# Optimization experiments

Hardware: AMD Instinct MI355X
Metric: run time of the kernel (lower is better)

The kernel has to match this reference:

```python
import jax, jax.numpy as jnp
import numpy as np

N = 100000      # nodes
E = 800000      # edges (avg degree 8)
F = 5           # num_node_features
D = 128         # embed_dim
H = 4           # heads
HD = D // H     # per-head dim = 32
H1, H2 = 64, 128  # mlp hidden dims


def _mlp(x, W1, b1, W2, b2, W3, b3):
    h = jax.nn.relu(x @ W1 + b1)
    h = jax.nn.relu(h @ W2 + b2)
    return h @ W3 + b3


def setup_inputs() -> dict:
    key = jax.random.key(0)
    ks = jax.random.split(key, 24)
    g = lambda i, shape: (jax.random.normal(ks[i], shape, dtype=jnp.float32) * 0.05)
    z = lambda d: jnp.zeros((d,), dtype=jnp.float32)
    return {
        "x": jax.random.normal(ks[0], (N, F), dtype=jnp.float32),
        "edge_index": jax.random.randint(ks[1], (2, E), 0, N),
        # mlp_prep: F -> 64 -> 128 -> D
        "prep_W1": g(2, (F, H1)),  "prep_b1": z(H1),
        "prep_W2": g(3, (H1, H2)), "prep_b2": z(H2),
        "prep_W3": g(4, (H2, D)),  "prep_b3": z(D),
        # mlp_update: D -> 64 -> 128 -> D
        "upd_W1": g(5, (D, H1)),   "upd_b1": z(H1),
        "upd_W2": g(6, (H1, H2)),  "upd_b2": z(H2),
        "upd_W3": g(7, (H2, D)),   "upd_b3": z(D),
        # TransformerConv projections (heads=4, per-head 32, concat -> D)
        "q_W": g(8, (D, D)),  "q_b": z(D),
        "k_W": g(9, (D, D)),  "k_b": z(D),
        "v_W": g(10, (D, D)), "v_b": z(D),
        "skip_W": g(11, (D, D)), "skip_b": z(D),
    }


def _transformer_conv(x, edge_index, q_W, q_b, k_W, k_b, v_W, v_b, skip_W, skip_b):
    # PyG TransformerConv: messages flow src=edge_index[0] -> dst=edge_index[1]
    src, dst = edge_index[0], edge_index[1]
    q = (x @ q_W + q_b).reshape(N, H, HD)
    k = (x @ k_W + k_b).reshape(N, H, HD)
    v = (x @ v_W + v_b).reshape(N, H, HD)
    scale = 1.0 / np.sqrt(HD).astype(np.float32)
    # per-edge attention logits [E, H]
    score = jnp.einsum('ehd,ehd->eh', q[dst], k[src]) * scale
    # segment softmax over incoming edges of each destination node
    m = jax.ops.segment_max(score, dst, num_segments=N)          # [N, H]
    e = jnp.exp(score - m[dst])                                  # [E, H]
    denom = jax.ops.segment_sum(e, dst, num_segments=N)         # [N, H]
    alpha = e / denom[dst]                                       # [E, H]
    # scatter-aggregate weighted values
    agg = jax.ops.segment_sum(alpha[..., None] * v[src], dst, num_segments=N)  # [N, H, HD]
    return agg.reshape(N, H * HD) + (x @ skip_W + skip_b)


def reference(x, edge_index,
              prep_W1, prep_b1, prep_W2, prep_b2, prep_W3, prep_b3,
              upd_W1, upd_b1, upd_W2, upd_b2, upd_W3, upd_b3,
              q_W, q_b, k_W, k_b, v_W, v_b, skip_W, skip_b):
    h_init = _mlp(x, prep_W1, prep_b1, prep_W2, prep_b2, prep_W3, prep_b3)
    h = _transformer_conv(h_init, edge_index, q_W, q_b, k_W, k_b, v_W, v_b, skip_W, skip_b)
    return h + _mlp(h, upd_W1, upd_b1, upd_W2, upd_b2, upd_W3, upd_b3)
```

## Files before the change

### kernel.cpp

```cpp
#include <hip/hip_runtime.h>
#include <hip/hip_bf16.h>

#define N_  100000
#define F_  5
#define D_  128
#define H_  4
#define HD_ 32
#define E_  800000

typedef __attribute__((ext_vector_type(8))) short bf16x8;
typedef __attribute__((ext_vector_type(4))) float f32x4;

__device__ __forceinline__ unsigned short f2bf(float f) {
  unsigned u = __float_as_uint(f);
  u += 0x7FFF + ((u >> 16) & 1);
  return (unsigned short)(u >> 16);
}

__device__ __forceinline__ unsigned pk2(float a, float b) {
  __hip_bfloat162 h = __float22bfloat162_rn(make_float2(a, b));
  return *(unsigned*)&h;
}

__device__ __forceinline__ float2 bf2f2(unsigned u) {
  float2 r;
  r.x = __uint_as_float(u << 16);
  r.y = __uint_as_float(u & 0xffff0000u);
  return r;
}

__device__ __forceinline__ float rowsum8(float x) {
  x += __int_as_float(__builtin_amdgcn_update_dpp(0, __float_as_int(x), 0x0B1, 0xF, 0xF, false));
  x += __int_as_float(__builtin_amdgcn_update_dpp(0, __float_as_int(x), 0x04E, 0xF, 0xF, false));
  x += __int_as_float(__builtin_amdgcn_update_dpp(0, __float_as_int(x), 0x141, 0xF, 0xF, false));
  return x;
}

template<int K, int M>
__device__ __forceinline__ void wconv_one(const float* __restrict__ W,
                                          unsigned short* __restrict__ WT,
                                          int idx) {
  const int r = idx & 7;
  const int l = (idx >> 3) & 15;
  const int rest = idx >> 7;
  const int kq = rest % (K / 8);
  const int i  = rest / (K / 8);
  WT[idx] = f2bf(W[(kq * 8 + r) * M + i * 16 + l]);
}

#define WCONV_NB 480
#define HIST_NB  ((E_ + 255) / 256)
#define SCAN_NB  ((N_ + 255) / 256)

__global__ __launch_bounds__(256) void k_wconv_hist(
    const float* __restrict__ w0, const float* __restrict__ w1,
    const float* __restrict__ w2, const float* __restrict__ w3,
    const float* __restrict__ w4, const float* __restrict__ w5,
    const float* __restrict__ w6, const float* __restrict__ w7,
    const float* __restrict__ w8, unsigned short* __restrict__ WT,
    const int* __restrict__ ei, int* __restrict__ deg)
{
  if (blockIdx.x >= WCONV_NB) {
    const int e = (blockIdx.x - WCONV_NB) * 256 + threadIdx.x;
    if (e < E_) atomicAdd(&deg[ei[E_ + e]], 1);
    return;
  }
  const int idx = blockIdx.x * 256 + threadIdx.x;
  if (idx < 8192)        wconv_one<64, 128>(w0, WT,          idx);
  else if (idx < 24576)  wconv_one<128,128>(w1, WT + 8192,   idx - 8192);
  else if (idx < 40960)  wconv_one<128,128>(w2, WT + 24576,  idx - 24576);
  else if (idx < 57344)  wconv_one<128,128>(w3, WT + 40960,  idx - 40960);
  else if (idx < 73728)  wconv_one<128,128>(w4, WT + 57344,  idx - 57344);
  else if (idx < 90112)  wconv_one<128,128>(w5, WT + 73728,  idx - 73728);
  else if (idx < 98304)  wconv_one<128, 64>(w6, WT + 90112,  idx - 90112);
  else if (idx < 106496) wconv_one<64, 128>(w7, WT + 98304,  idx - 98304);
  else                   wconv_one<128,128>(w8, WT + 106496, idx - 106496);
}

template<int K, int M>
__device__ __forceinline__ void gemm_frag64(const unsigned short* sX,
                                            const unsigned short* __restrict__ WT,
                                            f32x4 (*acc)[4],
                                            int wr, int l16, int kg)
{
  constexpr int SX = K + 8;
  constexpr int IF = M / 64;
  #pragma unroll
  for (int i = 0; i < IF; ++i)
    #pragma unroll
    for (int j = 0; j < 4; ++j) acc[i][j] = (f32x4){0.f, 0.f, 0.f, 0.f};
  #pragma unroll
  for (int k0 = 0; k0 < K; k0 += 32) {
    const int kq = k0 / 8 + kg;
    bf16x8 aw[IF];
    #pragma unroll
    for (int i = 0; i < IF; ++i)
      aw[i] = *(const bf16x8*)&WT[(((wr * IF + i) * (K / 8) + kq) * 16 + l16) * 8];
    #pragma unroll
    for (int j = 0; j < 4; ++j) {
      const bf16x8 bx = *(const bf16x8*)&sX[(j * 16 + l16) * SX + k0 + kg * 8];
      #pragma unroll
      for (int i = 0; i < IF; ++i)
        acc[i][j] = __builtin_amdgcn_mfma_f32_16x16x32_bf16(aw[i], bx, acc[i][j], 0, 0, 0);
    }
  }
}

template<int M, bool RELU, int SXO>
__device__ __forceinline__ void acc_to_lds64(unsigned short* sY, f32x4 (*acc)[4],
                                             const float* __restrict__ bias,
                                             int wr, int l16, int kg)
{
  constexpr int IF = M / 64;
  float4 b4[IF];
  #pragma unroll
  for (int i = 0; i < IF; ++i)
    b4[i] = *(const float4*)&bias[(wr * IF + i) * 16 + kg * 4];
  #pragma unroll
  for (int j = 0; j < 4; ++j) {
    const int row = j * 16 + l16;
    #pragma unroll
    for (int i = 0; i < IF; ++i) {
      const int f0 = (wr * IF + i) * 16 + kg * 4;
      float ox = acc[i][j][0] + b4[i].x, oy = acc[i][j][1] + b4[i].y;
      float oz = acc[i][j][2] + b4[i].z, ow = acc[i][j][3] + b4[i].w;
      if constexpr (RELU) {
        ox = fmaxf(ox, 0.f); oy = fmaxf(oy, 0.f);
        oz = fmaxf(oz, 0.f); ow = fmaxf(ow, 0.f);
      }
      uint2 p;
      p.x = pk2(ox, oy);
      p.y = pk2(oz, ow);
      *(uint2*)&sY[row * SXO + f0] = p;
    }
  }
}

__global__ __launch_bounds__(256) void k_scan1(const int* __restrict__ deg,
                                               int* __restrict__ off,
                                               int* __restrict__ bsum) {
  __shared__ int s[256];
  const int t = threadIdx.x;
  const int i = blockIdx.x * 256 + t;
  const int v = (i < N_) ? deg[i] : 0;
  s[t] = v;
  __syncthreads();
  #pragma unroll
  for (int o = 1; o < 256; o <<= 1) {
    int u = (t >= o) ? s[t - o] : 0;
    __syncthreads();
    s[t] += u;
    __syncthreads();
  }
  if (i < N_) off[i] = s[t] - v;
  if (t == 255) bsum[blockIdx.x] = s[255];
}

__global__ __launch_bounds__(256) void k_scan23(const int* __restrict__ off,
                                                const int* __restrict__ bsum,
                                                int* __restrict__ cur,
                                                const int* __restrict__ deg,
                                                int2* __restrict__ meta) {
  __shared__ int sacc[256];
  const int t = threadIdx.x;
  const int bid = blockIdx.x;
  int s = 0;
  for (int j = t; j < bid; j += 256) s += bsum[j];
  sacc[t] = s;
  __syncthreads();
  #pragma unroll
  for (int o = 128; o > 0; o >>= 1) {
    if (t < o) sacc[t] += sacc[t + o];
    __syncthreads();
  }
  const int prefix = sacc[0];
  const int i = bid * 256 + t;
  if (i < N_) {
    const int o = off[i] + prefix;
    cur[i] = o;
    meta[i] = make_int2(o, deg[i]);
  }
}

__global__ __launch_bounds__(256) void k_fill_prep(
    const int* __restrict__ ei, int* __restrict__ cur, int* __restrict__ esrc,
    const float* __restrict__ x,
    const float* __restrict__ pW1, const float* __restrict__ pb1,
    const unsigned short* __restrict__ wt_p2, const float* __restrict__ pb2,
    const unsigned short* __restrict__ wt_p3, const float* __restrict__ pb3,
    const unsigned short* __restrict__ wt_q, const float* __restrict__ qb,
    const unsigned short* __restrict__ wt_k, const float* __restrict__ kb,
    const unsigned short* __restrict__ wt_v, const float* __restrict__ vb,
    const unsigned short* __restrict__ wt_s, const float* __restrict__ sb,
    unsigned short* __restrict__ q16, unsigned short* __restrict__ k16,
    unsigned short* __restrict__ v16, float* __restrict__ out)
{
  __shared__ __align__(16) unsigned short bufA[64 * 72];
  __shared__ __align__(16) unsigned short bufB[64 * 136];

  const int bmod = blockIdx.x % 3;
  if (bmod != 2) {
    const int fid = (blockIdx.x / 3) * 2 + bmod;
    const int e = fid * 256 + threadIdx.x;
    if (e < E_) {
      const int src = ei[e], dst = ei[E_ + e];
      const int pos = atomicAdd(&cur[dst], 1);
      esrc[pos] = src;
    }
    return;
  }

  const int t = threadIdx.x;
  const int node0 = (blockIdx.x / 3) * 64;
  const int lane = t & 63;
  const int wr = t >> 6;
  const int l16 = lane & 15, kg = lane >> 4;

  float* sxs = (float*)bufB;
  float* sw1 = (float*)bufB + 320;
  {
    const long gbase = (long)node0 * F_;
    for (int i = t; i < 64 * F_; i += 256) {
      const long g = gbase + i;
      sxs[i] = (g < (long)N_ * F_) ? x[g] : 0.f;
    }
    for (int i = t; i < 384; i += 256)
      sw1[i] = (i < 320) ? pW1[i] : pb1[i - 320];
  }
  __syncthreads();

  {
    const int n = t >> 2;
    const int f0b = (t & 3) * 16;
    float xr[F_];
    #pragma unroll
    for (int k = 0; k < F_; ++k) xr[k] = sxs[n * F_ + k];
    const float* sb1 = sw1 + 320;
    #pragma unroll
    for (int q = 0; q < 4; ++q) {
      float o[4];
      #pragma unroll
      for (int jj = 0; jj < 4; ++jj) {
        const int f = f0b + q * 4 + jj;
        float a = sb1[f];
        #pragma unroll
        for (int k = 0; k < F_; ++k) a = fmaf(xr[k], sw1[k * 64 + f], a);
        o[jj] = fmaxf(a, 0.f);
      }
      uint2 pkd;
      pkd.x = pk2(o[0], o[1]);
      pkd.y = pk2(o[2], o[3]);
      *(uint2*)&bufA[n * 72 + f0b + q * 4] = pkd;
    }
  }
  __syncthreads();

  f32x4 acc[2][4];

  gemm_frag64<64, 128>(bufA, wt_p2, acc, wr, l16, kg);
  acc_to_lds64<128, true, 136>(bufB, acc, pb2, wr, l16, kg);
  __syncthreads();

  gemm_frag64<128, 128>(bufB, wt_p3, acc, wr, l16, kg);
  __syncthreads();
  acc_to_lds64<128, false, 136>(bufB, acc, pb3, wr, l16, kg);
  __syncthreads();

  {
    const unsigned short* wtsP[3] = {wt_q, wt_k, wt_v};
    const float* bsP[3] = {qb, kb, vb};
    unsigned short* ysP[3] = {q16, k16, v16};
    #pragma unroll
    for (int ws = 0; ws < 3; ++ws) {
      gemm_frag64<128, 128>(bufB, wtsP[ws], acc, wr, l16, kg);
      const float* __restrict__ bias = bsP[ws];
      unsigned short* __restrict__ Yb = ysP[ws];
      float4 b4[2];
      #pragma unroll
      for (int i = 0; i < 2; ++i)
        b4[i] = *(const float4*)&bias[(wr * 2 + i) * 16 + kg * 4];
      #pragma unroll
      for (int j = 0; j < 4; ++j) {
        const int node = node0 + j * 16 + l16;
        if (node >= N_) continue;
        #pragma unroll
        for (int i = 0; i < 2; ++i) {
          const int f0 = (wr * 2 + i) * 16 + kg * 4;
          uint2 ob;
          ob.x = pk2(acc[i][j][0] + b4[i].x, acc[i][j][1] + b4[i].y);
          ob.y = pk2(acc[i][j][2] + b4[i].z, acc[i][j][3] + b4[i].w);
          *(uint2*)&Yb[(long)node * D_ + f0] = ob;
        }
      }
    }
  }

  gemm_frag64<128, 128>(bufB, wt_s, acc, wr, l16, kg);
  {
    float4 b4[2];
    #pragma unroll
    for (int i = 0; i < 2; ++i)
      b4[i] = *(const float4*)&sb[(wr * 2 + i) * 16 + kg * 4];
    #pragma unroll
    for (int j = 0; j < 4; ++j) {
      const int node = node0 + j * 16 + l16;
      if (node >= N_) continue;
      #pragma unroll
      for (int i = 0; i < 2; ++i) {
        const int f0 = (wr * 2 + i) * 16 + kg * 4;
        float4 o = make_float4(acc[i][j][0] + b4[i].x, acc[i][j][1] + b4[i].y,
                               acc[i][j][2] + b4[i].z, acc[i][j][3] + b4[i].w);
        *(float4*)&out[(long)node * D_ + f0] = o;
      }
    }
  }
}

__global__ __launch_bounds__(256) void k_update(
    const unsigned short* __restrict__ wt_u1, const float* __restrict__ ub1,
    const unsigned short* __restrict__ wt_u2, const float* __restrict__ ub2,
    const unsigned short* __restrict__ wt_u3, const float* __restrict__ ub3,
    float* __restrict__ out)
{
  __shared__ __align__(16) unsigned short bufA[64 * 72];
  __shared__ __align__(16) unsigned short bufB[64 * 136];

  const int t = threadIdx.x;
  const int node0 = blockIdx.x * 64;
  const int lane = t & 63;
  const int wr = t >> 6;
  const int l16 = lane & 15, kg = lane >> 4;

  #pragma unroll
  for (int i = 0; i < 8; ++i) {
    const int g = t + 256 * i;
    const int row = g >> 5;
    const int kc  = g & 31;
    const int node = node0 + row;
    float4 xv = (node < N_) ? ((const float4*)out)[(long)node * 32 + kc]
                            : make_float4(0.f, 0.f, 0.f, 0.f);
    uint2 p;
    p.x = pk2(xv.x, xv.y);
    p.y = pk2(xv.z, xv.w);
    *(uint2*)&bufB[row * 136 + kc * 4] = p;
  }
  __syncthreads();

  f32x4 acc[2][4];

  gemm_frag64<128, 64>(bufB, wt_u1, acc, wr, l16, kg);
  acc_to_lds64<64, true, 72>(bufA, acc, ub1, wr, l16, kg);
  __syncthreads();

  gemm_frag64<64, 128>(bufA, wt_u2, acc, wr, l16, kg);
  acc_to_lds64<128, true, 136>(bufB, acc, ub2, wr, l16, kg);
  __syncthreads();

  gemm_frag64<128, 128>(bufB, wt_u3, acc, wr, l16, kg);
  {
    float4 b4[2];
    #pragma unroll
    for (int i = 0; i < 2; ++i)
      b4[i] = *(const float4*)&ub3[(wr * 2 + i) * 16 + kg * 4];
    #pragma unroll
    for (int j = 0; j < 4; ++j) {
      const int node = node0 + j * 16 + l16;
      if (node >= N_) continue;
      #pragma unroll
      for (int i = 0; i < 2; ++i) {
        const int f0 = (wr * 2 + i) * 16 + kg * 4;
        const float4 r = *(const float4*)&out[(long)node * D_ + f0];
        float4 o = make_float4(acc[i][j][0] + b4[i].x + r.x,
                               acc[i][j][1] + b4[i].y + r.y,
                               acc[i][j][2] + b4[i].z + r.z,
                               acc[i][j][3] + b4[i].w + r.w);
        *(float4*)&out[(long)node * D_ + f0] = o;
      }
    }
  }
}

__global__ __launch_bounds__(256) void k_attn(
    const int* __restrict__ esrc, const int2* __restrict__ meta,
    const unsigned short* __restrict__ q,
    const unsigned short* __restrict__ kbuf,
    const unsigned short* __restrict__ vbuf,
    float* __restrict__ out)
{
  const int t = threadIdx.x;
  const unsigned node = blockIdx.x * 8 + (t >> 5);
  const int c = t & 31;
  const float C = 0.17677669529663687f * 1.4426950408889634f;

  const int2 md = meta[node];
  const int start = md.x, cnt = md.y;
  const int end = start + cnt;

  const uint2 qu = *(const uint2*)&q[(node << 7) + 4u * c];
  const float2 q01 = bf2f2(qu.x), q23 = bf2f2(qu.y);
  const float qx0 = q01.x * C, qx1 = q01.y * C;
  const float qx2 = q23.x * C, qx3 = q23.y * C;

  float l = 0.f, a0 = 0.f, a1 = 0.f, a2 = 0.f, a3 = 0.f;

  const int P = (cnt + 1) >> 1;
  if (P > 0) {
    bool v1c = (start + 1) < end;
    unsigned i0 = esrc[start];
    unsigned i1 = esrc[v1c ? start + 1 : start];
    uint2 kA = *(const uint2*)&kbuf[((long)i0 << 7) + 4u * c];
    uint2 kB = *(const uint2*)&kbuf[((long)i1 << 7) + 4u * c];
    uint2 wA = *(const uint2*)&vbuf[((long)i0 << 7) + 4u * c];
    uint2 wB = *(const uint2*)&vbuf[((long)i1 << 7) + 4u * c];
    bool v0n = (start + 2) < end, v1n = (start + 3) < end;
    unsigned i0n = esrc[v0n ? start + 2 : start];
    unsigned i1n = esrc[v1n ? start + 3 : start];

    for (int it = 0;;) {
      const bool more = (it + 1) < P;
      uint2 kAn, kBn, wAn, wBn;
      unsigned i0f = 0, i1f = 0;
      bool v0f = false, v1f = false;
      if (more) {
        kAn = *(const uint2*)&kbuf[((long)i0n << 7) + 4u * c];
        kBn = *(const uint2*)&kbuf[((long)i1n << 7) + 4u * c];
        wAn = *(const uint2*)&vbuf[((long)i0n << 7) + 4u * c];
        wBn = *(const uint2*)&vbuf[((long)i1n << 7) + 4u * c];
        const int ef = start + 2 * (it + 2);
        v0f = ef < end; v1f = (ef + 1) < end;
        i0f = esrc[v0f ? ef : start];
        i1f = esrc[v1f ? ef + 1 : start];
      }

      const float2 ka01 = bf2f2(kA.x), ka23 = bf2f2(kA.y);
      const float2 kb01 = bf2f2(kB.x), kb23 = bf2f2(kB.y);
      float sA = fmaf(qx0, ka01.x, fmaf(qx1, ka01.y, fmaf(qx2, ka23.x, qx3 * ka23.y)));
      float sB = fmaf(qx0, kb01.x, fmaf(qx1, kb01.y, fmaf(qx2, kb23.x, qx3 * kb23.y)));
      sA = rowsum8(sA);
      sB = rowsum8(sB);
      const float eA = __builtin_amdgcn_exp2f(sA);
      const float eB = v1c ? __builtin_amdgcn_exp2f(sB) : 0.f;
      const float2 va01 = bf2f2(wA.x), va23 = bf2f2(wA.y);
      const float2 vb01 = bf2f2(wB.x), vb23 = bf2f2(wB.y);
      l += eA + eB;
      a0 = fmaf(eA, va01.x, fmaf(eB, vb01.x, a0));
      a1 = fmaf(eA, va01.y, fmaf(eB, vb01.y, a1));
      a2 = fmaf(eA, va23.x, fmaf(eB, vb23.x, a2));
      a3 = fmaf(eA, va23.y, fmaf(eB, vb23.y, a3));

      if (!more) break;
      ++it;
      kA = kAn; kB = kBn; wA = wAn; wB = wBn;
      v1c = v1n;
      v0n = v0f; v1n = v1f;
      i0n = i0f; i1n = i1f;
    }
  }

  if (l > 0.f) {
    const float inv = 1.0f / l;
    float4* op = (float4*)&out[(node << 7) + 4u * c];
    float4 cv = *op;
    cv.x += a0 * inv;
    cv.y += a1 * inv;
    cv.z += a2 * inv;
    cv.w += a3 * inv;
    *op = cv;
  }
}

extern "C" void kernel_launch(void* const* d_in, const int* in_sizes, int n_in,
                              void* d_out, int out_size, void* d_ws, size_t ws_size,
                              hipStream_t stream) {
  const float* x   = (const float*)d_in[0];
  const int*   ei  = (const int*)d_in[1];
  const float* pW1 = (const float*)d_in[2];  const float* pb1 = (const float*)d_in[3];
  const float* pW2 = (const float*)d_in[4];  const float* pb2 = (const float*)d_in[5];
  const float* pW3 = (const float*)d_in[6];  const float* pb3 = (const float*)d_in[7];
  const float* uW1 = (const float*)d_in[8];  const float* ub1 = (const float*)d_in[9];
  const float* uW2 = (const float*)d_in[10]; const float* ub2 = (const float*)d_in[11];
  const float* uW3 = (const float*)d_in[12]; const float* ub3 = (const float*)d_in[13];
  const float* qW  = (const float*)d_in[14]; const float* qb  = (const float*)d_in[15];
  const float* kW  = (const float*)d_in[16]; const float* kb  = (const float*)d_in[17];
  const float* vW  = (const float*)d_in[18]; const float* vb  = (const float*)d_in[19];
  const float* sW  = (const float*)d_in[20]; const float* sb  = (const float*)d_in[21];

  float* out = (float*)d_out;
  float* ws  = (float*)d_ws;

  const long ND = (long)N_ * D_;
  unsigned short* q16 = (unsigned short*)(ws + ND);
  unsigned short* k16 = (unsigned short*)(ws + 2 * ND);
  unsigned short* v16 = (unsigned short*)(ws + 3 * ND);

  unsigned short* wtb = (unsigned short*)(ws + 4 * ND);
  unsigned short* wt_p2 = wtb;
  unsigned short* wt_p3 = wtb + 8192;
  unsigned short* wt_q  = wtb + 24576;
  unsigned short* wt_k  = wtb + 40960;
  unsigned short* wt_v  = wtb + 57344;
  unsigned short* wt_s  = wtb + 73728;
  unsigned short* wt_u1 = wtb + 90112;
  unsigned short* wt_u2 = wtb + 98304;
  unsigned short* wt_u3 = wtb + 106496;

  int* deg  = (int*)ws;
  int* off  = deg + N_;
  int* cur  = off + N_;
  int* esrc = cur + N_;
  int* bsum = esrc + E_;
  int2* meta = (int2*)(bsum + 512);

  const int gT64 = (N_ + 63) / 64;

  hipMemsetAsync(deg, 0, N_ * sizeof(int), stream);

  k_wconv_hist<<<WCONV_NB + HIST_NB, 256, 0, stream>>>(
      pW2, pW3, qW, kW, vW, sW, uW1, uW2, uW3, wtb, ei, deg);

  k_scan1 <<<SCAN_NB, 256, 0, stream>>>(deg, off, bsum);
  k_scan23<<<SCAN_NB, 256, 0, stream>>>(off, bsum, cur, deg, meta);

  k_fill_prep<<<3 * gT64, 256, 0, stream>>>(
      ei, cur, esrc,
      x, pW1, pb1, wt_p2, pb2, wt_p3, pb3,
      wt_q, qb, wt_k, kb, wt_v, vb, wt_s, sb,
      q16, k16, v16, out);

  k_attn<<<N_ / 8, 256, 0, stream>>>(esrc, meta, q16, k16, v16, out);

  k_update<<<gT64, 256, 0, stream>>>(wt_u1, ub1, wt_u2, ub2, wt_u3, ub3, out);
}
```

Measured before the change: 314.9 us.

## Overlap attention tail with update MLP and write bf16 h for update

```diff
diff --git a/kernel.cpp b/kernel.cpp
--- a/kernel.cpp
+++ b/kernel.cpp
@@ -7,6 +7,8 @@
 #define H_  4
 #define HD_ 32
 #define E_  800000
+
+#define NA_ 50048
 
 typedef __attribute__((ext_vector_type(8))) short bf16x8;
 typedef __attribute__((ext_vector_type(4))) float f32x4;
@@ -182,8 +184,9 @@
   }
 }
 
-__global__ __launch_bounds__(256) void k_fill_prep(
-    const int* __restrict__ ei, int* __restrict__ cur, int* __restrict__ esrc,
+__device__ __forceinline__ void prep_body(
+    int node0, int t,
+    unsigned short* bufA, unsigned short* bufB,
     const float* __restrict__ x,
     const float* __restrict__ pW1, const float* __restrict__ pb1,
     const unsigned short* __restrict__ wt_p2, const float* __restrict__ pb2,
@@ -195,23 +198,6 @@
     unsigned short* __restrict__ q16, unsigned short* __restrict__ k16,
     unsigned short* __restrict__ v16, float* __restrict__ out)
 {
-  __shared__ __align__(16) unsigned short bufA[64 * 72];
-  __shared__ __align__(16) unsigned short bufB[64 * 136];
-
-  const int bmod = blockIdx.x % 3;
-  if (bmod != 2) {
-    const int fid = (blockIdx.x / 3) * 2 + bmod;
-    const int e = fid * 256 + threadIdx.x;
-    if (e < E_) {
-      const int src = ei[e], dst = ei[E_ + e];
-      const int pos = atomicAdd(&cur[dst], 1);
-      esrc[pos] = src;
-    }
-    return;
-  }
-
-  const int t = threadIdx.x;
-  const int node0 = (blockIdx.x / 3) * 64;
   const int lane = t & 63;
   const int wr = t >> 6;
   const int l16 = lane & 15, kg = lane >> 4;
@@ -316,87 +302,53 @@
   }
 }
 
-__global__ __launch_bounds__(256) void k_update(
-    const unsigned short* __restrict__ wt_u1, const float* __restrict__ ub1,
-    const unsigned short* __restrict__ wt_u2, const float* __restrict__ ub2,
-    const unsigned short* __restrict__ wt_u3, const float* __restrict__ ub3,
-    float* __restrict__ out)
+__global__ __launch_bounds__(256) void k_fill_prep(
+    const int* __restrict__ ei, int* __restrict__ cur, int* __restrict__ esrc,
+    const float* __restrict__ x,
+    const float* __restrict__ pW1, const float* __restrict__ pb1,
+    const unsigned short* __restrict__ wt_p2, const float* __restrict__ pb2,
+    const unsigned short* __restrict__ wt_p3, const float* __restrict__ pb3,
+    const unsigned short* __restrict__ wt_q, const float* __restrict__ qb,
+    const unsigned short* __restrict__ wt_k, const float* __restrict__ kb,
+    const unsigned short* __restrict__ wt_v, const float* __restrict__ vb,
+    const unsigned short* __restrict__ wt_s, const float* __restrict__ sb,
+    unsigned short* __restrict__ q16, unsigned short* __restrict__ k16,
+    unsigned short* __restrict__ v16, float* __restrict__ out)
 {
   __shared__ __align__(16) unsigned short bufA[64 * 72];
   __shared__ __align__(16) unsigned short bufB[64 * 136];
 
-  const int t = threadIdx.x;
-  const int node0 = blockIdx.x * 64;
-  const int lane = t & 63;
-  const int wr = t >> 6;
-  const int l16 = lane & 15, kg = lane >> 4;
-
-  #pragma unroll
-  for (int i = 0; i < 8; ++i) {
-    const int g = t + 256 * i;
-    const int row = g >> 5;
-    const int kc  = g & 31;
-    const int node = node0 + row;
-    float4 xv = (node < N_) ? ((const float4*)out)[(long)node * 32 + kc]
-                            : make_float4(0.f, 0.f, 0.f, 0.f);
-    uint2 p;
-    p.x = pk2(xv.x, xv.y);
-    p.y = pk2(xv.z, xv.w);
-    *(uint2*)&bufB[row * 136 + kc * 4] = p;
-  }
-  __syncthreads();
-
-  f32x4 acc[2][4];
-
-  gemm_frag64<128, 64>(bufB, wt_u1, acc, wr, l16, kg);
-  acc_to_lds64<64, true, 72>(bufA, acc, ub1, wr, l16, kg);
-  __syncthreads();
-
-  gemm_frag64<64, 128>(bufA, wt_u2, acc, wr, l16, kg);
-  acc_to_lds64<128, true, 136>(bufB, acc, ub2, wr, l16, kg);
-  __syncthreads();
-
-  gemm_frag64<128, 128>(bufB, wt_u3, acc, wr, l16, kg);
-  {
-    float4 b4[2];
-    #pragma unroll
-    for (int i = 0; i < 2; ++i)
-      b4[i] = *(const float4*)&ub3[(wr * 2 + i) * 16 + kg * 4];
-    #pragma unroll
-    for (int j = 0; j < 4; ++j) {
-      const int node = node0 + j * 16 + l16;
-      if (node >= N_) continue;
-      #pragma unroll
-      for (int i = 0; i < 2; ++i) {
-        const int f0 = (wr * 2 + i) * 16 + kg * 4;
-        const float4 r = *(const float4*)&out[(long)node * D_ + f0];
-        float4 o = make_float4(acc[i][j][0] + b4[i].x + r.x,
-                               acc[i][j][1] + b4[i].y + r.y,
-                               acc[i][j][2] + b4[i].z + r.z,
-                               acc[i][j][3] + b4[i].w + r.w);
-        *(float4*)&out[(long)node * D_ + f0] = o;
-      }
-    }
-  }
-}
-
-__global__ __launch_bounds__(256) void k_attn(
+  const int bmod = blockIdx.x % 3;
+  if (bmod != 2) {
+    const int fid = (blockIdx.x / 3) * 2 + bmod;
+    const int e = fid * 256 + threadIdx.x;
+    if (e < E_) {
+      const int src = ei[e], dst = ei[E_ + e];
+      const int pos = atomicAdd(&cur[dst], 1);
+      esrc[pos] = src;
+    }
+    return;
+  }
+  prep_body((blockIdx.x / 3) * 64, threadIdx.x, bufA, bufB,
+            x, pW1, pb1, wt_p2, pb2, wt_p3, pb3,
+            wt_q, qb, wt_k, kb, wt_v, vb, wt_s, sb,
+            q16, k16, v16, out);
+}
+
+__device__ __forceinline__ void attn_node(
+    unsigned node, int c,
     const int* __restrict__ esrc, const int2* __restrict__ meta,
-    const unsigned short* __restrict__ q,
+    unsigned short* __restrict__ q16,
     const unsigned short* __restrict__ kbuf,
     const unsigned short* __restrict__ vbuf,
     float* __restrict__ out)
 {
-  const int t = threadIdx.x;
-  const unsigned node = blockIdx.x * 8 + (t >> 5);
-  const int c = t & 31;
   const float C = 0.17677669529663687f * 1.4426950408889634f;
-
   const int2 md = meta[node];
   const int start = md.x, cnt = md.y;
   const int end = start + cnt;
 
-  const uint2 qu = *(const uint2*)&q[(node << 7) + 4u * c];
+  const uint2 qu = *(const uint2*)&q16[((long)node << 7) + 4u * c];
   const float2 q01 = bf2f2(qu.x), q23 = bf2f2(qu.y);
   const float qx0 = q01.x * C, qx1 = q01.y * C;
   const float qx2 = q23.x * C, qx3 = q23.y * C;
@@ -457,16 +409,131 @@
     }
   }
 
+  float r0 = 0.f, r1 = 0.f, r2 = 0.f, r3 = 0.f;
   if (l > 0.f) {
     const float inv = 1.0f / l;
-    float4* op = (float4*)&out[(node << 7) + 4u * c];
-    float4 cv = *op;
-    cv.x += a0 * inv;
-    cv.y += a1 * inv;
-    cv.z += a2 * inv;
-    cv.w += a3 * inv;
-    *op = cv;
-  }
+    r0 = a0 * inv; r1 = a1 * inv; r2 = a2 * inv; r3 = a3 * inv;
+  }
+
+  float4* op = (float4*)&out[((long)node << 7) + 4u * c];
+  float4 sk = *op;
+  const float h0 = sk.x + r0, h1 = sk.y + r1;
+  const float h2 = sk.z + r2, h3 = sk.w + r3;
+  *op = make_float4(h0, h1, h2, h3);
+  uint2 hb;
+  hb.x = pk2(h0, h1);
+  hb.y = pk2(h2, h3);
+  *(uint2*)&q16[((long)node << 7) + 4u * c] = hb;
+}
+
+__global__ __launch_bounds__(256) void k_attn(
+    const int* __restrict__ esrc, const int2* __restrict__ meta,
+    unsigned short* __restrict__ q16,
+    const unsigned short* __restrict__ kbuf,
+    const unsigned short* __restrict__ vbuf,
+    float* __restrict__ out, int node0)
+{
+  const int t = threadIdx.x;
+  attn_node(node0 + blockIdx.x * 8 + (t >> 5), t & 31,
+            esrc, meta, q16, kbuf, vbuf, out);
+}
+
+__device__ __forceinline__ void update_body(
+    int node0, int t,
+    unsigned short* bufA, unsigned short* bufB,
+    const unsigned short* __restrict__ h16,
+    const unsigned short* __restrict__ wt_u1, const float* __restrict__ ub1,
+    const unsigned short* __restrict__ wt_u2, const float* __restrict__ ub2,
+    const unsigned short* __restrict__ wt_u3, const float* __restrict__ ub3,
+    float* __restrict__ out)
+{
+  const int lane = t & 63;
+  const int wr = t >> 6;
+  const int l16 = lane & 15, kg = lane >> 4;
+
+  #pragma unroll
+  for (int i = 0; i < 4; ++i) {
+    const int g = t + 256 * i;
+    const int row = g >> 4;
+    const int kc  = g & 15;
+    const int node = node0 + row;
+    uint4 v = (node < N_) ? *(const uint4*)&h16[((long)node << 7) + kc * 8]
+                          : make_uint4(0u, 0u, 0u, 0u);
+    *(uint4*)&bufB[row * 136 + kc * 8] = v;
+  }
+  __syncthreads();
+
+  f32x4 acc[2][4];
+
+  gemm_frag64<128, 64>(bufB, wt_u1, acc, wr, l16, kg);
+  acc_to_lds64<64, true, 72>(bufA, acc, ub1, wr, l16, kg);
+  __syncthreads();
+
+  gemm_frag64<64, 128>(bufA, wt_u2, acc, wr, l16, kg);
+  acc_to_lds64<128, true, 136>(bufB, acc, ub2, wr, l16, kg);
+  __syncthreads();
+
+  gemm_frag64<128, 128>(bufB, wt_u3, acc, wr, l16, kg);
+  {
+    float4 b4[2];
+    #pragma unroll
+    for (int i = 0; i < 2; ++i)
+      b4[i] = *(const float4*)&ub3[(wr * 2 + i) * 16 + kg * 4];
+    #pragma unroll
+    for (int j = 0; j < 4; ++j) {
+      const int node = node0 + j * 16 + l16;
+      if (node >= N_) continue;
+      #pragma unroll
+      for (int i = 0; i < 2; ++i) {
+        const int f0 = (wr * 2 + i) * 16 + kg * 4;
+        const float4 r = *(const float4*)&out[(long)node * D_ + f0];
+        float4 o = make_float4(acc[i][j][0] + b4[i].x + r.x,
+                               acc[i][j][1] + b4[i].y + r.y,
+                               acc[i][j][2] + b4[i].z + r.z,
+                               acc[i][j][3] + b4[i].w + r.w);
+        *(float4*)&out[(long)node * D_ + f0] = o;
+      }
+    }
+  }
+}
+
+__global__ __launch_bounds__(256) void k_attnB_updA(
+    const int* __restrict__ esrc, const int2* __restrict__ meta,
+    unsigned short* __restrict__ q16,
+    const unsigned short* __restrict__ kbuf,
+    const unsigned short* __restrict__ vbuf,
+    const unsigned short* __restrict__ wt_u1, const float* __restrict__ ub1,
+    const unsigned short* __restrict__ wt_u2, const float* __restrict__ ub2,
+    const unsigned short* __restrict__ wt_u3, const float* __restrict__ ub3,
+    float* __restrict__ out)
+{
+  __shared__ __align__(16) unsigned short bufA[64 * 72];
+  __shared__ __align__(16) unsigned short bufB[64 * 136];
+
+  const int bid = blockIdx.x;
+  const int t = threadIdx.x;
+  if (bid % 9 == 8) {
+    update_body((bid / 9) * 64, t, bufA, bufB, q16,
+                wt_u1, ub1, wt_u2, ub2, wt_u3, ub3, out);
+    return;
+  }
+  const int aid = (bid / 9) * 8 + (bid % 9);
+  if (aid >= (N_ - NA_) / 8) return;
+  attn_node(NA_ + aid * 8 + (t >> 5), t & 31,
+            esrc, meta, q16, kbuf, vbuf, out);
+}
+
+__global__ __launch_bounds__(256) void k_update(
+    const unsigned short* __restrict__ h16,
+    const unsigned short* __restrict__ wt_u1, const float* __restrict__ ub1,
+    const unsigned short* __restrict__ wt_u2, const float* __restrict__ ub2,
+    const unsigned short* __restrict__ wt_u3, const float* __restrict__ ub3,
+    float* __restrict__ out, int node0)
+{
+  __shared__ __align__(16) unsigned short bufA[64 * 72];
+  __shared__ __align__(16) unsigned short bufB[64 * 136];
+  update_body(node0 + blockIdx.x * 64, threadIdx.x, bufA, bufB, h16,
+              wt_u1, ub1, wt_u2, ub2, wt_u3, ub3, out);
 }
 
 extern "C" void kernel_launch(void* const* d_in, const int* in_sizes, int n_in,
@@ -527,7 +594,12 @@
       wt_q, qb, wt_k, kb, wt_v, vb, wt_s, sb,
       q16, k16, v16, out);
 
-  k_attn<<<N_ / 8, 256, 0, stream>>>(esrc, meta, q16, k16, v16, out);
-
-  k_update<<<gT64, 256, 0, stream>>>(wt_u1, ub1, wt_u2, ub2, wt_u3, ub3, out);
-}
+  k_attn<<<NA_ / 8, 256, 0, stream>>>(esrc, meta, q16, k16, v16, out, 0);
+
+  k_attnB_updA<<<9 * (NA_ / 64), 256, 0, stream>>>(
+      esrc, meta, q16, k16, v16,
+      wt_u1, ub1, wt_u2, ub2, wt_u3, ub3, out);
+
+  k_update<<<(N_ - NA_ + 63) / 64, 256, 0, stream>>>(
+      q16, wt_u1, ub1, wt_u2, ub2, wt_u3, ub3, out, NA_);
+}
```

Result: no change. 319.0 us (+1.3%).

## Spread prep MLP tiles across scan kernels and pass bf16 h to update

Applied to the files above, without the earlier changes.

```diff
diff --git a/kernel.cpp b/kernel.cpp
--- a/kernel.cpp
+++ b/kernel.cpp
@@ -51,6 +51,8 @@
 #define WCONV_NB 480
 #define HIST_NB  ((E_ + 255) / 256)
 #define SCAN_NB  ((N_ + 255) / 256)
+#define PREP_NT  1563
+#define PREP_CH  521
 
 __global__ __launch_bounds__(256) void k_wconv_hist(
     const float* __restrict__ w0, const float* __restrict__ w1,
@@ -136,54 +138,9 @@
   }
 }
 
-__global__ __launch_bounds__(256) void k_scan1(const int* __restrict__ deg,
-                                               int* __restrict__ off,
-                                               int* __restrict__ bsum) {
-  __shared__ int s[256];
-  const int t = threadIdx.x;
-  const int i = blockIdx.x * 256 + t;
-  const int v = (i < N_) ? deg[i] : 0;
-  s[t] = v;
-  __syncthreads();
-  #pragma unroll
-  for (int o = 1; o < 256; o <<= 1) {
-    int u = (t >= o) ? s[t - o] : 0;
-    __syncthreads();
-    s[t] += u;
-    __syncthreads();
-  }
-  if (i < N_) off[i] = s[t] - v;
-  if (t == 255) bsum[blockIdx.x] = s[255];
-}
-
-__global__ __launch_bounds__(256) void k_scan23(const int* __restrict__ off,
-                                                const int* __restrict__ bsum,
-                                                int* __restrict__ cur,
-                                                const int* __restrict__ deg,
-                                                int2* __restrict__ meta) {
-  __shared__ int sacc[256];
-  const int t = threadIdx.x;
-  const int bid = blockIdx.x;
-  int s = 0;
-  for (int j = t; j < bid; j += 256) s += bsum[j];
-  sacc[t] = s;
-  __syncthreads();
-  #pragma unroll
-  for (int o = 128; o > 0; o >>= 1) {
-    if (t < o) sacc[t] += sacc[t + o];
-    __syncthreads();
-  }
-  const int prefix = sacc[0];
-  const int i = bid * 256 + t;
-  if (i < N_) {
-    const int o = off[i] + prefix;
-    cur[i] = o;
-    meta[i] = make_int2(o, deg[i]);
-  }
-}
-
-__global__ __launch_bounds__(256) void k_fill_prep(
-    const int* __restrict__ ei, int* __restrict__ cur, int* __restrict__ esrc,
+__device__ __forceinline__ void prep_body(
+    int node0, int t,
+    unsigned short* bufA, unsigned short* bufB,
     const float* __restrict__ x,
     const float* __restrict__ pW1, const float* __restrict__ pb1,
     const unsigned short* __restrict__ wt_p2, const float* __restrict__ pb2,
@@ -195,23 +152,6 @@
     unsigned short* __restrict__ q16, unsigned short* __restrict__ k16,
     unsigned short* __restrict__ v16, float* __restrict__ out)
 {
-  __shared__ __align__(16) unsigned short bufA[64 * 72];
-  __shared__ __align__(16) unsigned short bufB[64 * 136];
-
-  const int bmod = blockIdx.x % 3;
-  if (bmod != 2) {
-    const int fid = (blockIdx.x / 3) * 2 + bmod;
-    const int e = fid * 256 + threadIdx.x;
-    if (e < E_) {
-      const int src = ei[e], dst = ei[E_ + e];
-      const int pos = atomicAdd(&cur[dst], 1);
-      esrc[pos] = src;
-    }
-    return;
-  }
-
-  const int t = threadIdx.x;
-  const int node0 = (blockIdx.x / 3) * 64;
   const int lane = t & 63;
   const int wr = t >> 6;
   const int l16 = lane & 15, kg = lane >> 4;
@@ -316,73 +256,109 @@
   }
 }
 
-__global__ __launch_bounds__(256) void k_update(
-    const unsigned short* __restrict__ wt_u1, const float* __restrict__ ub1,
-    const unsigned short* __restrict__ wt_u2, const float* __restrict__ ub2,
-    const unsigned short* __restrict__ wt_u3, const float* __restrict__ ub3,
-    float* __restrict__ out)
+#define PREP_ARGS                                                        \
+    const float* __restrict__ x,                                         \
+    const float* __restrict__ pW1, const float* __restrict__ pb1,        \
+    const unsigned short* __restrict__ wt_p2, const float* __restrict__ pb2, \
+    const unsigned short* __restrict__ wt_p3, const float* __restrict__ pb3, \
+    const unsigned short* __restrict__ wt_q, const float* __restrict__ qb,   \
+    const unsigned short* __restrict__ wt_k, const float* __restrict__ kb,   \
+    const unsigned short* __restrict__ wt_v, const float* __restrict__ vb,   \
+    const unsigned short* __restrict__ wt_s, const float* __restrict__ sb,   \
+    unsigned short* __restrict__ q16, unsigned short* __restrict__ k16,  \
+    unsigned short* __restrict__ v16, float* __restrict__ out
+
+#define PREP_PASS x, pW1, pb1, wt_p2, pb2, wt_p3, pb3, wt_q, qb, wt_k, kb, \
+                  wt_v, vb, wt_s, sb, q16, k16, v16, out
+
+__global__ __launch_bounds__(256) void k_scan1_prep(
+    const int* __restrict__ deg, int* __restrict__ off, int* __restrict__ bsum,
+    PREP_ARGS)
 {
   __shared__ __align__(16) unsigned short bufA[64 * 72];
   __shared__ __align__(16) unsigned short bufB[64 * 136];
+  __shared__ int s[256];
 
   const int t = threadIdx.x;
-  const int node0 = blockIdx.x * 64;
-  const int lane = t & 63;
-  const int wr = t >> 6;
-  const int l16 = lane & 15, kg = lane >> 4;
-
-  #pragma unroll
-  for (int i = 0; i < 8; ++i) {
-    const int g = t + 256 * i;
-    const int row = g >> 5;
-    const int kc  = g & 31;
-    const int node = node0 + row;
-    float4 xv = (node < N_) ? ((const float4*)out)[(long)node * 32 + kc]
-                            : make_float4(0.f, 0.f, 0.f, 0.f);
-    uint2 p;
-    p.x = pk2(xv.x, xv.y);
-    p.y = pk2(xv.z, xv.w);
-    *(uint2*)&bufB[row * 136 + kc * 4] = p;
-  }
-  __syncthreads();
-
-  f32x4 acc[2][4];
-
-  gemm_frag64<128, 64>(bufB, wt_u1, acc, wr, l16, kg);
-  acc_to_lds64<64, true, 72>(bufA, acc, ub1, wr, l16, kg);
-  __syncthreads();
-
-  gemm_frag64<64, 128>(bufA, wt_u2, acc, wr, l16, kg);
-  acc_to_lds64<128, true, 136>(bufB, acc, ub2, wr, l16, kg);
-  __syncthreads();
-
-  gemm_frag64<128, 128>(bufB, wt_u3, acc, wr, l16, kg);
-  {
-    float4 b4[2];
-    #pragma unroll
-    for (int i = 0; i < 2; ++i)
-      b4[i] = *(const float4*)&ub3[(wr * 2 + i) * 16 + kg * 4];
-    #pragma unroll
-    for (int j = 0; j < 4; ++j) {
-      const int node = node0 + j * 16 + l16;
-      if (node >= N_) continue;
-      #pragma unroll
-      for (int i = 0; i < 2; ++i) {
-        const int f0 = (wr * 2 + i) * 16 + kg * 4;
-        const float4 r = *(const float4*)&out[(long)node * D_ + f0];
-        float4 o = make_float4(acc[i][j][0] + b4[i].x + r.x,
-                               acc[i][j][1] + b4[i].y + r.y,
-                               acc[i][j][2] + b4[i].z + r.z,
-                               acc[i][j][3] + b4[i].w + r.w);
-        *(float4*)&out[(long)node * D_ + f0] = o;
-      }
-    }
-  }
+  if (blockIdx.x < SCAN_NB) {
+    const int i = blockIdx.x * 256 + t;
+    const int v = (i < N_) ? deg[i] : 0;
+    s[t] = v;
+    __syncthreads();
+    #pragma unroll
+    for (int o = 1; o < 256; o <<= 1) {
+      int u = (t >= o) ? s[t - o] : 0;
+      __syncthreads();
+      s[t] += u;
+      __syncthreads();
+    }
+    if (i < N_) off[i] = s[t] - v;
+    if (t == 255) bsum[blockIdx.x] = s[255];
+    return;
+  }
+  prep_body((blockIdx.x - SCAN_NB) * 64, t, bufA, bufB, PREP_PASS);
+}
+
+__global__ __launch_bounds__(256) void k_scan23_prep(
+    const int* __restrict__ off, const int* __restrict__ bsum,
+    int* __restrict__ cur, const int* __restrict__ deg,
+    int2* __restrict__ meta, PREP_ARGS)
+{
+  __shared__ __align__(16) unsigned short bufA[64 * 72];
+  __shared__ __align__(16) unsigned short bufB[64 * 136];
+  __shared__ int sacc[256];
+
+  const int t = threadIdx.x;
+  if (blockIdx.x < SCAN_NB) {
+    const int bid = blockIdx.x;
+    int s = 0;
+    for (int j = t; j < bid; j += 256) s += bsum[j];
+    sacc[t] = s;
+    __syncthreads();
+    #pragma unroll
+    for (int o = 128; o > 0; o >>= 1) {
+      if (t < o) sacc[t] += sacc[t + o];
+      __syncthreads();
+    }
+    const int prefix = sacc[0];
+    const int i = bid * 256 + t;
+    if (i < N_) {
+      const int o = off[i] + prefix;
+      cur[i] = o;
+      meta[i] = make_int2(o, deg[i]);
+    }
+    return;
+  }
+  prep_body((PREP_CH + blockIdx.x - SCAN_NB) * 64, t, bufA, bufB, PREP_PASS);
+}
+
+__global__ __launch_bounds__(256) void k_fill_prep(
+    const int* __restrict__ ei, int* __restrict__ cur, int* __restrict__ esrc,
+    PREP_ARGS)
+{
+  __shared__ __align__(16) unsigned short bufA[64 * 72];
+  __shared__ __align__(16) unsigned short bufB[64 * 136];
+
+  const int t = threadIdx.x;
+  const int bmod = blockIdx.x % 7;
+  if (bmod != 6) {
+    const int fid = (blockIdx.x / 7) * 6 + bmod;
+    const int e = fid * 256 + t;
+    if (e < E_) {
+      const int src = ei[e], dst = ei[E_ + e];
+      const int pos = atomicAdd(&cur[dst], 1);
+      esrc[pos] = src;
+    }
+    return;
+  }
+  const int tile = 2 * PREP_CH + blockIdx.x / 7;
+  if (tile >= PREP_NT) return;
+  prep_body(tile * 64, t, bufA, bufB, PREP_PASS);
 }
 
 __global__ __launch_bounds__(256) void k_attn(
     const int* __restrict__ esrc, const int2* __restrict__ meta,
-    const unsigned short* __restrict__ q,
+    unsigned short* __restrict__ q16,
     const unsigned short* __restrict__ kbuf,
     const unsigned short* __restrict__ vbuf,
     float* __restrict__ out)
@@ -396,7 +372,7 @@
   const int start = md.x, cnt = md.y;
   const int end = start + cnt;
 
-  const uint2 qu = *(const uint2*)&q[(node << 7) + 4u * c];
+  const uint2 qu = *(const uint2*)&q16[((long)node << 7) + 4u * c];
   const float2 q01 = bf2f2(qu.x), q23 = bf2f2(qu.y);
   const float qx0 = q01.x * C, qx1 = q01.y * C;
   const float qx2 = q23.x * C, qx3 = q23.y * C;
@@ -457,15 +433,82 @@
     }
   }
 
+  float r0 = 0.f, r1 = 0.f, r2 = 0.f, r3 = 0.f;
   if (l > 0.f) {
     const float inv = 1.0f / l;
-    float4* op = (float4*)&out[(node << 7) + 4u * c];
-    float4 cv = *op;
-    cv.x += a0 * inv;
-    cv.y += a1 * inv;
-    cv.z += a2 * inv;
-    cv.w += a3 * inv;
-    *op = cv;
+    r0 = a0 * inv; r1 = a1 * inv; r2 = a2 * inv; r3 = a3 * inv;
+  }
+
+  float4* op = (float4*)&out[((long)node << 7) + 4u * c];
+  float4 sk = *op;
+  const float h0 = sk.x + r0, h1 = sk.y + r1;
+  const float h2 = sk.z + r2, h3 = sk.w + r3;
+  *op = make_float4(h0, h1, h2, h3);
+  uint2 hb;
+  hb.x = pk2(h0, h1);
+  hb.y = pk2(h2, h3);
+  *(uint2*)&q16[((long)node << 7) + 4u * c] = hb;
+}
+
+__global__ __launch_bounds__(256) void k_update(
+    const unsigned short* __restrict__ h16,
+    const unsigned short* __restrict__ wt_u1, const float* __restrict__ ub1,
+    const unsigned short* __restrict__ wt_u2, const float* __restrict__ ub2,
+    const unsigned short* __restrict__ wt_u3, const float* __restrict__ ub3,
+    float* __restrict__ out)
+{
+  __shared__ __align__(16) unsigned short bufA[64 * 72];
+  __shared__ __align__(16) unsigned short bufB[64 * 136];
+
+  const int t = threadIdx.x;
+  const int node0 = blockIdx.x * 64;
+  const int lane = t & 63;
+  const int wr = t >> 6;
+  const int l16 = lane & 15, kg = lane >> 4;
+
+  #pragma unroll
+  for (int i = 0; i < 4; ++i) {
+    const int g = t + 256 * i;
+    const int row = g >> 4;
+    const int kc  = g & 15;
+    const int node = node0 + row;
+    uint4 v = (node < N_) ? *(const uint4*)&h16[((long)node << 7) + kc * 8]
+                          : make_uint4(0u, 0u, 0u, 0u);
+    *(uint4*)&bufB[row * 136 + kc * 8] = v;
+  }
+  __syncthreads();
+
+  f32x4 acc[2][4];
+
+  gemm_frag64<128, 64>(bufB, wt_u1, acc, wr, l16, kg);
+  acc_to_lds64<64, true, 72>(bufA, acc, ub1, wr, l16, kg);
+  __syncthreads();
+
+  gemm_frag64<64, 128>(bufA, wt_u2, acc, wr, l16, kg);
+  acc_to_lds64<128, true, 136>(bufB, acc, ub2, wr, l16, kg);
+  __syncthreads();
+
+  gemm_frag64<128, 128>(bufB, wt_u3, acc, wr, l16, kg);
+  {
+    float4 b4[2];
+    #pragma unroll
+    for (int i = 0; i < 2; ++i)
+      b4[i] = *(const float4*)&ub3[(wr * 2 + i) * 16 + kg * 4];
+    #pragma unroll
+    for (int j = 0; j < 4; ++j) {
+      const int node = node0 + j * 16 + l16;
+      if (node >= N_) continue;
+      #pragma unroll
+      for (int i = 0; i < 2; ++i) {
+        const int f0 = (wr * 2 + i) * 16 + kg * 4;
+        const float4 r = *(const float4*)&out[(long)node * D_ + f0];
+        float4 o = make_float4(acc[i][j][0] + b4[i].x + r.x,
+                               acc[i][j][1] + b4[i].y + r.y,
+                               acc[i][j][2] + b4[i].z + r.z,
+                               acc[i][j][3] + b4[i].w + r.w);
+        *(float4*)&out[(long)node * D_ + f0] = o;
+      }
+    }
   }
 }
 
@@ -511,17 +554,24 @@
   int* bsum = esrc + E_;
   int2* meta = (int2*)(bsum + 512);
 
-  const int gT64 = (N_ + 63) / 64;
-
   hipMemsetAsync(deg, 0, N_ * sizeof(int), stream);
 
   k_wconv_hist<<<WCONV_NB + HIST_NB, 256, 0, stream>>>(
       pW2, pW3, qW, kW, vW, sW, uW1, uW2, uW3, wtb, ei, deg);
 
-  k_scan1 <<<SCAN_NB, 256, 0, stream>>>(deg, off, bsum);
-  k_scan23<<<SCAN_NB, 256, 0, stream>>>(off, bsum, cur, deg, meta);
-
-  k_fill_prep<<<3 * gT64, 256, 0, stream>>>(
+  k_scan1_prep<<<SCAN_NB + PREP_CH, 256, 0, stream>>>(
+      deg, off, bsum,
+      x, pW1, pb1, wt_p2, pb2, wt_p3, pb3,
+      wt_q, qb, wt_k, kb, wt_v, vb, wt_s, sb,
+      q16, k16, v16, out);
+
+  k_scan23_prep<<<SCAN_NB + PREP_CH, 256, 0, stream>>>(
+      off, bsum, cur, deg, meta,
+      x, pW1, pb1, wt_p2, pb2, wt_p3, pb3,
+      wt_q, qb, wt_k, kb, wt_v, vb, wt_s, sb,
+      q16, k16, v16, out);
+
+  k_fill_prep<<<7 * (PREP_CH + 1), 256, 0, stream>>>(
       ei, cur, esrc,
       x, pW1, pb1, wt_p2, pb2, wt_p3, pb3,
       wt_q, qb, wt_k, kb, wt_v, vb, wt_s, sb,
@@ -529,5 +579,6 @@
 
   k_attn<<<N_ / 8, 256, 0, stream>>>(esrc, meta, q16, k16, v16, out);
 
-  k_update<<<gT64, 256, 0, stream>>>(wt_u1, ub1, wt_u2, ub2, wt_u3, ub3, out);
-}
+  k_update<<<PREP_NT, 256, 0, stream>>>(
+      q16, wt_u1, ub1, wt_u2, ub2, wt_u3, ub3, out);
+}
```

New measurement: 345.8 us. 9.8% more time.
